# Kernel tuning notes

Hardware: AMD Instinct MI355X
Metric: run time of the kernel (lower is better)

The kernel has to match this reference:

```python
import jax, jax.numpy as jnp
import numpy as np

N = 100000
E = 800000
D_IN = 128
D_H = 128
D_OUT = 40
L = 16
ALPHA = 0.1
THETA = 0.5
BN_EPS = 1e-5


def setup_inputs() -> dict:
    key = jax.random.key(0)
    ks = jax.random.split(key, 8)
    x = jax.random.normal(ks[0], (N, D_IN), dtype=jnp.float32)
    edge_row = jax.random.randint(ks[1], (E,), 0, N, dtype=jnp.int32)
    edge_col = jax.random.randint(ks[2], (E,), 0, N, dtype=jnp.int32)
    edge_weight = jax.random.uniform(ks[3], (E,), dtype=jnp.float32) / 8.0  # ~normalized adj values
    W_in = jax.random.normal(ks[4], (D_IN, D_H), dtype=jnp.float32) / np.sqrt(D_IN)
    b_in = jnp.zeros((D_H,), jnp.float32)
    conv_W = jax.random.normal(ks[5], (L, D_H, D_H), dtype=jnp.float32) / np.sqrt(D_H)
    bn_gamma = jnp.ones((L, D_H), jnp.float32)
    bn_beta = jnp.zeros((L, D_H), jnp.float32)
    W_out = jax.random.normal(ks[6], (D_H, D_OUT), dtype=jnp.float32) / np.sqrt(D_H)
    b_out = jnp.zeros((D_OUT,), jnp.float32)
    return {"x": x, "edge_weight": edge_weight, "W_in": W_in, "b_in": b_in,
            "conv_W": conv_W, "bn_gamma": bn_gamma, "bn_beta": bn_beta,
            "W_out": W_out, "b_out": b_out,
            "edge_row": edge_row, "edge_col": edge_col}


def reference(x, edge_weight, W_in, b_in, conv_W, bn_gamma, bn_beta, W_out, b_out, edge_row, edge_col):
    # input linear + relu (dropout p=0 -> identity)
    x0 = jax.nn.relu(x @ W_in + b_in)            # [N, D_H]
    # GCN2Conv beta coefficients: log(theta/layer + 1), layer = 1..L
    betas = jnp.log(THETA / jnp.arange(1, L + 1, dtype=jnp.float32) + 1.0)

    def spmm(h):
        # out[i] = sum_{e: row[e]=i} w[e] * h[col[e]]
        msgs = edge_weight[:, None] * h[edge_col]     # [E, D_H]
        return jax.ops.segment_sum(msgs, edge_row, num_segments=N)

    def layer(h, params):
        W, g, bb, beta = params
        a = spmm(h)                                   # propagate
        a = (1.0 - ALPHA) * a + ALPHA * x0            # initial-residual mix
        a = (1.0 - beta) * a + beta * (a @ W)         # shared-weights identity mapping
        mu = jnp.mean(a, axis=0)                      # BatchNorm1d (training stats)
        var = jnp.var(a, axis=0)
        a = (a - mu) * jax.lax.rsqrt(var + BN_EPS) * g + bb
        a = a + h                                     # residual
        return jax.nn.relu(a), None

    xL, _ = jax.lax.scan(layer, x0, (conv_W, bn_gamma, bn_beta, betas))
    return xL @ W_out + b_out                         # [N, D_OUT]
```

## Files before the change

### kernel.cpp

```cpp
#include <hip/hip_runtime.h>
#include <math.h>

#define NN 100000
#define EE 800000
#define DH 128
#define NL 16
#define GEMM_GRID 1563
#define SG_GRID 782
#define NSLOT 32
#define WROWS 12500

typedef __bf16 bf16x8 __attribute__((ext_vector_type(8)));
typedef float f32x4 __attribute__((ext_vector_type(4)));

__global__ void k_hist(const int* __restrict__ row, int* __restrict__ cnt) {
    int e = blockIdx.x * 256 + threadIdx.x;
    if (e < EE) atomicAdd(&cnt[row[e]], 1);
}

__global__ void k_scan1(const int* __restrict__ cnt, int* __restrict__ rp, int* __restrict__ part) {
    __shared__ int buf[512];
    int tid = threadIdx.x;
    int i = blockIdx.x * 512 + tid;
    int v = (i < NN) ? cnt[i] : 0;
    buf[tid] = v;
    __syncthreads();
    for (int off = 1; off < 512; off <<= 1) {
        int x = (tid >= off) ? buf[tid - off] : 0;
        __syncthreads();
        buf[tid] += x;
        __syncthreads();
    }
    if (i < NN) rp[i] = buf[tid] - v;
    if (tid == 511) part[blockIdx.x] = buf[511];
}

__global__ void k_scan2(int* __restrict__ part, int nparts) {
    __shared__ int buf[256];
    int tid = threadIdx.x;
    int v = (tid < nparts) ? part[tid] : 0;
    buf[tid] = v;
    __syncthreads();
    for (int off = 1; off < 256; off <<= 1) {
        int x = (tid >= off) ? buf[tid - off] : 0;
        __syncthreads();
        buf[tid] += x;
        __syncthreads();
    }
    if (tid < nparts) part[tid] = buf[tid] - v;
}

__global__ void k_scan3(int* __restrict__ rp, const int* __restrict__ part) {
    int i = blockIdx.x * 512 + threadIdx.x;
    if (i < NN) rp[i] += part[blockIdx.x];
    if (i == 0) rp[NN] = EE;
}

__global__ void k_dhist(const int* __restrict__ cnt, int* __restrict__ dbin) {
    __shared__ int lb[64];
    int tid = threadIdx.x;
    if (tid < 64) lb[tid] = 0;
    __syncthreads();
    int i = blockIdx.x * 256 + tid;
    if (i < NN) {
        int d = cnt[i];
        if (d > 63) d = 63;
        atomicAdd(&lb[63 - d], 1);
    }
    __syncthreads();
    if (tid < 64 && lb[tid]) atomicAdd(&dbin[tid], lb[tid]);
}

__global__ void k_pscan(const int* __restrict__ dbin, int* __restrict__ dpre) {
    if (threadIdx.x == 0) {
        int s = 0;
        for (int i = 0; i < 64; ++i) { dpre[i] = s; s += dbin[i]; }
    }
}

__global__ void k_pscatter(const int* __restrict__ cnt, const int* __restrict__ dpre,
                           int* __restrict__ dfil, int* __restrict__ perm) {
    __shared__ int lcnt[64], lbase[64];
    int tid = threadIdx.x;
    if (tid < 64) lcnt[tid] = 0;
    __syncthreads();
    int i = blockIdx.x * 256 + tid;
    int b = 0, loc = 0;
    bool ok = (i < NN);
    if (ok) {
        int d = cnt[i];
        if (d > 63) d = 63;
        b = 63 - d;
        loc = atomicAdd(&lcnt[b], 1);
    }
    __syncthreads();
    if (tid < 64 && lcnt[tid]) lbase[tid] = atomicAdd(&dfil[tid], lcnt[tid]);
    __syncthreads();
    if (ok) perm[dpre[b] + lbase[b] + loc] = i;
}

__global__ void k_iperm(const int* __restrict__ perm, const int* __restrict__ cnt,
                        int* __restrict__ iperm, int* __restrict__ cnt2) {
    int i = blockIdx.x * 256 + threadIdx.x;
    if (i < NN) {
        int p = perm[i];
        iperm[p] = i;
        cnt2[i] = cnt[p];
    }
}

__global__ void k_fill(const int* __restrict__ row, const int* __restrict__ col,
                       const float* __restrict__ w, const int* __restrict__ rp,
                       const int* __restrict__ iperm,
                       int* __restrict__ fil, int2* __restrict__ ep) {
    int b = blockIdx.x;
    int win = b & 7;
    int e = (b >> 3) * 256 + threadIdx.x;
    if (e >= EE) return;
    int r = iperm[row[e]];
    if (r / WROWS != win) return;
    int pos = rp[r] + atomicAdd(&fil[r], 1);
    ep[pos] = make_int2(iperm[col[e]], __float_as_int(0.9f * w[e]));
}

__global__ void k_prep_w(const float* __restrict__ convW, const float* __restrict__ Win,
                         __bf16* __restrict__ Bhi, __bf16* __restrict__ Blo) {
    int l = blockIdx.x;
    const float* W;
    float beta, ob;
    if (l < NL) {
        beta = logf(0.5f / (float)(l + 1) + 1.0f);
        ob = 1.0f - beta;
        W = convW + (size_t)l * DH * DH;
    } else {
        beta = 1.0f;
        ob = 0.0f;
        W = Win;
    }
    __bf16* bh = Bhi + (size_t)l * DH * DH;
    __bf16* bl = Blo + (size_t)l * DH * DH;
    for (int i = threadIdx.x; i < DH * DH; i += 256) {
        int k = i >> 7, j = i & 127;
        float v = beta * W[i] + ((k == j) ? ob : 0.f);
        __bf16 hv = (__bf16)v;
        int t = j >> 4, n = j & 15, ks = k >> 5, quad = (k >> 3) & 3, e = k & 7;
        int off = ((t * 4 + ks) * 64 + quad * 16 + n) * 8 + e;
        bh[off] = hv;
        bl[off] = (__bf16)(v - (float)hv);
    }
}

__global__ void k_prep_out(const float* __restrict__ Wout, __bf16* __restrict__ Bhi, __bf16* __restrict__ Blo) {
    for (int i = threadIdx.x; i < DH * 48; i += 256) {
        int k = i / 48, j = i % 48;
        float v = (j < 40) ? Wout[k * 40 + j] : 0.f;
        __bf16 hv = (__bf16)v;
        int t = j >> 4, n = j & 15, ks = k >> 5, quad = (k >> 3) & 3, e = k & 7;
        int off = ((t * 4 + ks) * 64 + quad * 16 + n) * 8 + e;
        Bhi[off] = hv;
        Blo[off] = (__bf16)(v - (float)hv);
    }
}

__device__ inline void split8(const float* p, bf16x8& hi, bf16x8& lo) {
    f32x4 v0 = *(const f32x4*)p;
    f32x4 v1 = *(const f32x4*)(p + 4);
#pragma unroll
    for (int j = 0; j < 4; ++j) {
        __bf16 h0 = (__bf16)v0[j];
        hi[j] = h0;
        lo[j] = (__bf16)(v0[j] - (float)h0);
        __bf16 h1 = (__bf16)v1[j];
        hi[4 + j] = h1;
        lo[4 + j] = (__bf16)(v1[j] - (float)h1);
    }
}

#define MFMA(a, b, c) __builtin_amdgcn_mfma_f32_16x16x32_bf16(a, b, c, 0, 0, 0)

__device__ inline float dec_scale(unsigned int sc4, int ks) {
    return __uint_as_float(((sc4 >> (8 * ks)) & 0xffu) << 23);
}

#define DEC_DW(dw, wsv, a0, a1, a2, a3)                         \
    {                                                           \
        a0 = fmaf(wsv, (float)((dw)&0xffu), a0);                \
        a1 = fmaf(wsv, (float)(((dw) >> 8) & 0xffu), a1);       \
        a2 = fmaf(wsv, (float)(((dw) >> 16) & 0xffu), a2);      \
        a3 = fmaf(wsv, (float)((dw) >> 24), a3);                \
    }

#define EDGE_FMA(S4, W, RA, RB)                                       \
    {                                                                 \
        float _w = (W);                                               \
        float _w0 = _w * dec_scale(S4, 0);                            \
        float _w1 = _w * dec_scale(S4, 1);                            \
        float _w2 = _w * dec_scale(S4, 2);                            \
        float _w3 = _w * dec_scale(S4, 3);                            \
        sw0 += _w0; sw1 += _w1; sw2 += _w2; sw3 += _w3;               \
        DEC_DW((RA).x, _w0, acc[0][0], acc[0][1], acc[0][2], acc[0][3]); \
        DEC_DW((RA).y, _w0, acc[0][4], acc[0][5], acc[0][6], acc[0][7]); \
        DEC_DW((RA).z, _w1, acc[1][0], acc[1][1], acc[1][2], acc[1][3]); \
        DEC_DW((RA).w, _w1, acc[1][4], acc[1][5], acc[1][6], acc[1][7]); \
        DEC_DW((RB).x, _w2, acc[2][0], acc[2][1], acc[2][2], acc[2][3]); \
        DEC_DW((RB).y, _w2, acc[2][4], acc[2][5], acc[2][6], acc[2][7]); \
        DEC_DW((RB).z, _w3, acc[3][0], acc[3][1], acc[3][2], acc[3][3]); \
        DEC_DW((RB).w, _w3, acc[3][4], acc[3][5], acc[3][6], acc[3][7]); \
    }

__global__ void k_cvt8(const __bf16* __restrict__ src, unsigned char* __restrict__ q8,
                       unsigned char* __restrict__ sc) {
    int t = blockIdx.x * 256 + threadIdx.x;
    if (t >= NN * 4) return;
    int node = t >> 2, ks = t & 3;
    const __bf16* p = src + (size_t)node * DH + ks * 32;
    float v[32];
    float mx = 0.f;
#pragma unroll
    for (int i = 0; i < 4; ++i) {
        bf16x8 b = *(const bf16x8*)(p + i * 8);
#pragma unroll
        for (int c = 0; c < 8; ++c) {
            float f = (float)b[c];
            v[i * 8 + c] = f;
            mx = fmaxf(mx, fabsf(f));
        }
    }
    unsigned int em = (__float_as_uint(mx) >> 23) & 0xffu;
    unsigned int eb;
    float sinv;
    if (em < 7) { eb = 0; sinv = 0.f; }
    else { eb = em - 6; sinv = __uint_as_float((254 - eb) << 23); }
    sc[(size_t)node * 4 + ks] = (unsigned char)eb;
    unsigned char* bp = q8 + (size_t)node * 128 + (ks >> 1) * 64 + (ks & 1) * 8;
#pragma unroll
    for (int q = 0; q < 4; ++q) {
        uint2 w;
        w.x = 0; w.y = 0;
#pragma unroll
        for (int c = 0; c < 4; ++c) {
            unsigned int q0 = (unsigned int)rintf(fminf(fmaf(v[q * 8 + c], sinv, 128.f), 255.f));
            unsigned int q1 = (unsigned int)rintf(fminf(fmaf(v[q * 8 + 4 + c], sinv, 128.f), 255.f));
            w.x |= q0 << (8 * c);
            w.y |= q1 << (8 * c);
        }
        *(uint2*)(bp + q * 16) = w;
    }
}

__global__ __launch_bounds__(512, 4) void k_spmm_gemm(const unsigned char* __restrict__ hin8,
                                                      const unsigned char* __restrict__ hinsc,
                                                      const unsigned char* __restrict__ x08,
                                                      const unsigned char* __restrict__ x0sc,
                                                      const int* __restrict__ rp, const int2* __restrict__ ep,
                                                      __bf16* __restrict__ aout,
                                                      const __bf16* __restrict__ Bhi, const __bf16* __restrict__ Blo,
                                                      float* __restrict__ stats32) {
    __shared__ __bf16 Bs[2 * DH * DH];
    __shared__ float red[2][8][DH];
    int tid = threadIdx.x;
    {
        const f32x4* sh = (const f32x4*)Bhi;
        const f32x4* sl = (const f32x4*)Blo;
        f32x4* dh = (f32x4*)Bs;
        f32x4* dl = (f32x4*)(Bs + DH * DH);
#pragma unroll
        for (int i = 0; i < 4; ++i) {
            dh[tid + i * 512] = sh[tid + i * 512];
            dl[tid + i * 512] = sl[tid + i * 512];
        }
    }

    int wave = tid >> 6, lane = tid & 63;
    int n = lane & 15, quad = lane >> 4;
    int r0 = blockIdx.x * 128 + wave * 16;
    int node = r0 + n;
    int nc = (node < NN) ? node : (NN - 1);

    float acc[4][8];
#pragma unroll
    for (int ks = 0; ks < 4; ++ks)
#pragma unroll
        for (int c = 0; c < 8; ++c) acc[ks][c] = 0.f;
    float sw0 = 0.f, sw1 = 0.f, sw2 = 0.f, sw3 = 0.f;

    unsigned xs4 = *(const unsigned*)&x0sc[(size_t)nc * 4];
    const unsigned char* xb = x08 + (size_t)nc * 128 + quad * 16;
    uint4 xa = *(const uint4*)xb;
    uint4 xc = *(const uint4*)(xb + 64);

    int s = 0, e = 0;
    if (node < NN) { s = rp[node]; e = rp[node + 1]; }
    int cnt = e - s;
    int npairs = cnt >> 1;

    const unsigned char* hb = hin8 + quad * 16;

    int2 cP0, cP1, fP0, fP1;
    unsigned cS0, cS1;
    uint4 cA0, cB0, cA1, cB1;
    if (npairs > 0) {
        cP0 = ep[s]; cP1 = ep[s + 1];
        cS0 = *(const unsigned*)&hinsc[(size_t)cP0.x * 4];
        cS1 = *(const unsigned*)&hinsc[(size_t)cP1.x * 4];
        const unsigned char* b0 = hb + (size_t)cP0.x * 128;
        const unsigned char* b1 = hb + (size_t)cP1.x * 128;
        cA0 = *(const uint4*)b0; cB0 = *(const uint4*)(b0 + 64);
        cA1 = *(const uint4*)b1; cB1 = *(const uint4*)(b1 + 64);
        int jf = s + 2; if (jf > EE - 2) jf = EE - 2;
        fP0 = ep[jf]; fP1 = ep[jf + 1];
    }

    EDGE_FMA(xs4, 0.1f, xa, xc);

    int j = s;
    for (int it = 0; it < npairs; ++it) {
        int j2 = j + 4; if (j2 > EE - 2) j2 = EE - 2;
        int2 eN0 = ep[j2], eN1 = ep[j2 + 1];
        unsigned tS0 = *(const unsigned*)&hinsc[(size_t)fP0.x * 4];
        unsigned tS1 = *(const unsigned*)&hinsc[(size_t)fP1.x * 4];
        const unsigned char* b0 = hb + (size_t)fP0.x * 128;
        const unsigned char* b1 = hb + (size_t)fP1.x * 128;
        uint4 tA0 = *(const uint4*)b0, tB0 = *(const uint4*)(b0 + 64);
        uint4 tA1 = *(const uint4*)b1, tB1 = *(const uint4*)(b1 + 64);
        EDGE_FMA(cS0, __int_as_float(cP0.y), cA0, cB0);
        EDGE_FMA(cS1, __int_as_float(cP1.y), cA1, cB1);
        cP0 = fP0; cP1 = fP1; fP0 = eN0; fP1 = eN1;
        cS0 = tS0; cS1 = tS1;
        cA0 = tA0; cB0 = tB0; cA1 = tA1; cB1 = tB1;
        j += 2;
    }
    if (cnt & 1) {
        int2 pe = ep[e - 1];
        unsigned s4 = *(const unsigned*)&hinsc[(size_t)pe.x * 4];
        const unsigned char* bp = hb + (size_t)pe.x * 128;
        uint4 ra = *(const uint4*)bp, rb = *(const uint4*)(bp + 64);
        EDGE_FMA(s4, __int_as_float(pe.y), ra, rb);
    }

    bf16x8 av[4];
    {
        float sws[4] = {sw0, sw1, sw2, sw3};
#pragma unroll
        for (int ks = 0; ks < 4; ++ks)
#pragma unroll
            for (int c = 0; c < 8; ++c)
                av[ks][c] = (__bf16)(acc[ks][c] - 128.0f * sws[ks]);
    }

    __syncthreads();

    f32x4 gacc[8];
#pragma unroll
    for (int t = 0; t < 8; ++t) gacc[t] = (f32x4){0.f, 0.f, 0.f, 0.f};

#pragma unroll
    for (int ks = 0; ks < 4; ++ks) {
#pragma unroll
        for (int t = 0; t < 8; ++t) {
            int base = ((t * 4 + ks) * 64 + lane) * 8;
            bf16x8 bh = *(const bf16x8*)&Bs[base];
            bf16x8 bl = *(const bf16x8*)&Bs[DH * DH + base];
            gacc[t] = MFMA(av[ks], bh, gacc[t]);
            gacc[t] = MFMA(av[ks], bl, gacc[t]);
        }
    }

#pragma unroll
    for (int t = 0; t < 8; ++t) {
        float sm = 0.f, qq = 0.f;
#pragma unroll
        for (int r = 0; r < 4; ++r) {
            int row = r0 + quad * 4 + r;
            float v = gacc[t][r];
            if (row < NN) {
                aout[(size_t)row * DH + t * 16 + n] = (__bf16)v;
                sm += v;
                qq += v * v;
            }
        }
        sm += __shfl_xor(sm, 16); sm += __shfl_xor(sm, 32);
        qq += __shfl_xor(qq, 16); qq += __shfl_xor(qq, 32);
        if (quad == 0) {
            red[0][wave][t * 16 + n] = sm;
            red[1][wave][t * 16 + n] = qq;
        }
    }
    __syncthreads();
    if (tid < 256) {
        int which = tid >> 7, jj = tid & 127;
        float tot = 0.f;
#pragma unroll
        for (int w = 0; w < 8; ++w) tot += red[which][w][jj];
        atomicAdd(&stats32[(size_t)(blockIdx.x & (NSLOT - 1)) * 256 + tid], tot);
    }
}

__global__ __launch_bounds__(512, 4) void k_lin_in(const float* __restrict__ X, const int* __restrict__ perm,
                                                   const __bf16* __restrict__ Bhi, const __bf16* __restrict__ Blo,
                                                   const float* __restrict__ bin, __bf16* __restrict__ x0) {
    __shared__ __bf16 Bs[2 * DH * DH];
    int tid = threadIdx.x;
    {
        const f32x4* sh = (const f32x4*)Bhi;
        const f32x4* sl = (const f32x4*)Blo;
        f32x4* dh = (f32x4*)Bs;
        f32x4* dl = (f32x4*)(Bs + DH * DH);
#pragma unroll
        for (int i = 0; i < 4; ++i) {
            dh[tid + i * 512] = sh[tid + i * 512];
            dl[tid + i * 512] = sl[tid + i * 512];
        }
    }
    __syncthreads();

    int wave = tid >> 6, lane = tid & 63;
    int n = lane & 15, quad = lane >> 4;
    int r0 = blockIdx.x * 128 + wave * 16;
    int arow = r0 + n;
    if (arow > NN - 1) arow = NN - 1;
    const float* pa = X + (size_t)perm[arow] * DH + quad * 8;

    f32x4 acc[8];
#pragma unroll
    for (int t = 0; t < 8; ++t) acc[t] = (f32x4){0.f, 0.f, 0.f, 0.f};

#pragma unroll
    for (int ks = 0; ks < 4; ++ks) {
        bf16x8 ah, al;
        split8(pa + ks * 32, ah, al);
#pragma unroll
        for (int t = 0; t < 8; ++t) {
            int base = ((t * 4 + ks) * 64 + lane) * 8;
            bf16x8 bh = *(const bf16x8*)&Bs[base];
            bf16x8 bl = *(const bf16x8*)&Bs[DH * DH + base];
            acc[t] = MFMA(ah, bh, acc[t]);
            acc[t] = MFMA(al, bh, acc[t]);
            acc[t] = MFMA(ah, bl, acc[t]);
        }
    }

#pragma unroll
    for (int t = 0; t < 8; ++t) {
        float bj = bin[t * 16 + n];
#pragma unroll
        for (int r = 0; r < 4; ++r) {
            int row = r0 + quad * 4 + r;
            if (row < NN) {
                float v = fmaxf(acc[t][r] + bj, 0.f);
                x0[(size_t)row * DH + t * 16 + n] = (__bf16)v;
            }
        }
    }
}

__global__ __launch_bounds__(256) void k_gemm_out(const __bf16* __restrict__ A, const int* __restrict__ perm,
                                                  const __bf16* __restrict__ Bhi, const __bf16* __restrict__ Blo,
                                                  const float* __restrict__ bout, float* __restrict__ out) {
    __shared__ __bf16 Bs[2 * 48 * DH];
    int tid = threadIdx.x;
    {
        const f32x4* sh = (const f32x4*)Bhi;
        const f32x4* sl = (const f32x4*)Blo;
        f32x4* dh = (f32x4*)Bs;
        f32x4* dl = (f32x4*)(Bs + 48 * DH);
#pragma unroll
        for (int i = 0; i < 3; ++i) {
            dh[tid + i * 256] = sh[tid + i * 256];
            dl[tid + i * 256] = sl[tid + i * 256];
        }
    }
    __syncthreads();

    int wave = tid >> 6, lane = tid & 63;
    int n = lane & 15, quad = lane >> 4;
    int r0 = blockIdx.x * 64 + wave * 16;
    int arow = r0 + n;
    if (arow > NN - 1) arow = NN - 1;
    const __bf16* pa = A + (size_t)arow * DH + quad * 8;

    f32x4 acc[3];
#pragma unroll
    for (int t = 0; t < 3; ++t) acc[t] = (f32x4){0.f, 0.f, 0.f, 0.f};

#pragma unroll
    for (int ks = 0; ks < 4; ++ks) {
        bf16x8 av = *(const bf16x8*)(pa + ks * 32);
#pragma unroll
        for (int t = 0; t < 3; ++t) {
            int base = ((t * 4 + ks) * 64 + lane) * 8;
            bf16x8 bh = *(const bf16x8*)&Bs[base];
            bf16x8 bl = *(const bf16x8*)&Bs[48 * DH + base];
            acc[t] = MFMA(av, bh, acc[t]);
            acc[t] = MFMA(av, bl, acc[t]);
        }
    }

    int prow[4];
#pragma unroll
    for (int r = 0; r < 4; ++r) {
        int row = r0 + quad * 4 + r;
        prow[r] = (row < NN) ? perm[row] : 0;
    }

#pragma unroll
    for (int t = 0; t < 3; ++t) {
        int j = t * 16 + n;
        float bj = (j < 40) ? bout[j] : 0.f;
#pragma unroll
        for (int r = 0; r < 4; ++r) {
            int row = r0 + quad * 4 + r;
            if (row < NN && j < 40) out[(size_t)prow[r] * 40 + j] = acc[t][r] + bj;
        }
    }
}

__global__ __launch_bounds__(256) void k_update(const __bf16* __restrict__ a, const __bf16* __restrict__ hin,
                                                __bf16* __restrict__ hout,
                                                unsigned char* __restrict__ h8, unsigned char* __restrict__ hsc,
                                                const float* __restrict__ stats32,
                                                const float* __restrict__ gamma, const float* __restrict__ bbeta) {
    __shared__ float scb[DH], shb[DH];
    int tid = threadIdx.x;
    if (tid < DH) {
        float s = 0.f, q = 0.f;
#pragma unroll
        for (int sl = 0; sl < NSLOT; ++sl) {
            s += stats32[(size_t)sl * 256 + tid];
            q += stats32[(size_t)sl * 256 + 128 + tid];
        }
        float mu = s * (1.0f / NN);
        float var = q * (1.0f / NN) - mu * mu;
        if (var < 0.f) var = 0.f;
        float sc = gamma[tid] * rsqrtf(var + 1e-5f);
        scb[tid] = sc;
        shb[tid] = bbeta[tid] - mu * sc;
    }
    __syncthreads();

    int idx = blockIdx.x * 256 + tid;
    int sub = idx & 15;
    int j0 = sub * 8;
    bf16x8 av = ((const bf16x8*)a)[idx];
    bf16x8 hv = ((const bf16x8*)hin)[idx];
    bf16x8 o;
    float vv[8];
    float mx = 0.f;
#pragma unroll
    for (int c = 0; c < 8; ++c) {
        int j = j0 + c;
        float v = fmaxf(fmaf((float)av[c], scb[j], shb[j]) + (float)hv[c], 0.f);
        vv[c] = v;
        mx = fmaxf(mx, v);
        o[c] = (__bf16)v;
    }
    ((bf16x8*)hout)[idx] = o;

    mx = fmaxf(mx, __shfl_xor(mx, 1));
    mx = fmaxf(mx, __shfl_xor(mx, 2));
    unsigned int em = (__float_as_uint(mx) >> 23) & 0xffu;
    unsigned int eb;
    float sinv;
    if (em < 7) { eb = 0; sinv = 0.f; }
    else { eb = em - 6; sinv = __uint_as_float((254 - eb) << 23); }
    if ((tid & 3) == 0) hsc[(size_t)(idx >> 4) * 4 + (sub >> 2)] = (unsigned char)eb;
    uint2 pk;
    pk.x = 0; pk.y = 0;
#pragma unroll
    for (int c = 0; c < 4; ++c) {
        unsigned int q0 = (unsigned int)rintf(fminf(fmaf(vv[c], sinv, 128.f), 255.f));
        unsigned int q1 = (unsigned int)rintf(fminf(fmaf(vv[4 + c], sinv, 128.f), 255.f));
        pk.x |= q0 << (8 * c);
        pk.y |= q1 << (8 * c);
    }
    unsigned wpos = ((sub >> 3) & 1) * 64 + (sub & 3) * 16 + ((sub >> 2) & 1) * 8;
    *(uint2*)&h8[(size_t)(idx >> 4) * 128 + wpos] = pk;
}

extern "C" void kernel_launch(void* const* d_in, const int* in_sizes, int n_in,
                              void* d_out, int out_size, void* d_ws, size_t ws_size,
                              hipStream_t stream) {
    const float* x = (const float*)d_in[0];
    const float* ew = (const float*)d_in[1];
    const float* Win = (const float*)d_in[2];
    const float* bin = (const float*)d_in[3];
    const float* convW = (const float*)d_in[4];
    const float* gamma = (const float*)d_in[5];
    const float* bbeta = (const float*)d_in[6];
    const float* Wout = (const float*)d_in[7];
    const float* bout = (const float*)d_in[8];
    const int* erow = (const int*)d_in[9];
    const int* ecol = (const int*)d_in[10];
    float* out = (float*)d_out;

    char* wsp = (char*)d_ws;
    size_t off = 0;
    auto alloc = [&](size_t bytes) -> void* {
        void* p = wsp + off;
        off += (bytes + 255) & ~(size_t)255;
        return p;
    };
    __bf16* x0 = (__bf16*)alloc((size_t)NN * DH * 2);
    __bf16* h = (__bf16*)alloc((size_t)NN * DH * 2);
    __bf16* a = (__bf16*)alloc((size_t)NN * DH * 2);
    unsigned char* x08 = (unsigned char*)alloc((size_t)NN * DH);
    unsigned char* h8 = (unsigned char*)alloc((size_t)NN * DH);
    unsigned char* x0sc = (unsigned char*)alloc((size_t)NN * 4);
    unsigned char* hsc = (unsigned char*)alloc((size_t)NN * 4);
    int* rp = (int*)alloc((NN + 1) * 4);
    int* perm = (int*)alloc((size_t)NN * 4);
    int* iperm = (int*)alloc((size_t)NN * 4);
    int* cnt2 = (int*)alloc((size_t)NN * 4);
    int* dpre = (int*)alloc(64 * 4);
    size_t zero_bytes = (size_t)NN * 4 + (size_t)NN * 4 + (size_t)NL * NSLOT * 256 * 4 + 128 * 4;
    int* cnt = (int*)alloc(zero_bytes);
    int* fil = cnt + NN;
    float* stats32 = (float*)(fil + NN);
    int* dbin = (int*)(stats32 + (size_t)NL * NSLOT * 256);
    int* dfil = dbin + 64;
    int2* ep = (int2*)alloc((size_t)EE * 8);
    int* part = (int*)alloc(256 * 4);
    __bf16* Bhi = (__bf16*)alloc((size_t)(NL + 1) * DH * DH * 2);
    __bf16* Blo = (__bf16*)alloc((size_t)(NL + 1) * DH * DH * 2);
    __bf16* Bohi = (__bf16*)alloc((size_t)DH * 48 * 2);
    __bf16* Bolo = (__bf16*)alloc((size_t)DH * 48 * 2);

    hipMemsetAsync(cnt, 0, zero_bytes, stream);

    k_hist<<<3125, 256, 0, stream>>>(erow, cnt);
    k_dhist<<<391, 256, 0, stream>>>(cnt, dbin);
    k_pscan<<<1, 64, 0, stream>>>(dbin, dpre);
    k_pscatter<<<391, 256, 0, stream>>>(cnt, dpre, dfil, perm);
    k_iperm<<<391, 256, 0, stream>>>(perm, cnt, iperm, cnt2);
    k_scan1<<<196, 512, 0, stream>>>(cnt2, rp, part);
    k_scan2<<<1, 256, 0, stream>>>(part, 196);
    k_scan3<<<196, 512, 0, stream>>>(rp, part);
    k_fill<<<25000, 256, 0, stream>>>(erow, ecol, ew, rp, iperm, fil, ep);

    k_prep_w<<<NL + 1, 256, 0, stream>>>(convW, Win, Bhi, Blo);
    k_prep_out<<<1, 256, 0, stream>>>(Wout, Bohi, Bolo);

    k_lin_in<<<SG_GRID, 512, 0, stream>>>(x, perm, Bhi + (size_t)NL * DH * DH, Blo + (size_t)NL * DH * DH, bin, x0);
    k_cvt8<<<1563, 256, 0, stream>>>(x0, x08, x0sc);

    for (int l = 0; l < NL; ++l) {
        const unsigned char* hin8 = (l == 0) ? x08 : h8;
        const unsigned char* hinsc = (l == 0) ? x0sc : hsc;
        const __bf16* hin = (l == 0) ? x0 : h;
        float* st = stats32 + (size_t)l * NSLOT * 256;
        k_spmm_gemm<<<SG_GRID, 512, 0, stream>>>(hin8, hinsc, x08, x0sc, rp, ep, a,
                                                 Bhi + (size_t)l * DH * DH, Blo + (size_t)l * DH * DH, st);
        k_update<<<6250, 256, 0, stream>>>(a, hin, h, h8, hsc, st, gamma + l * DH, bbeta + l * DH);
    }
    k_gemm_out<<<GEMM_GRID, 256, 0, stream>>>(h, perm, Bohi, Bolo, bout, out);
}
```

Before: 1.154 ms.

## Store intermediate activations as 8-bit quantized, fuse x0 quantization, simplify edge fill

The spmm+gemm kernel now writes its per-layer output as 8-bit block-scaled values with per-32-column exponent scales instead of bf16, and the update kernel dequantizes them. This halves the intermediate write and read traffic every layer. The input linear kernel now quantizes x0 directly, so the separate conversion kernel is removed. The edge fill drops its 8-window row partitioning in favour of a single pass with nontemporal loads and stores. The extra quantization adds error to the pre-BatchNorm activations, though the statistics are still computed from full-precision values.

```diff
diff --git a/kernel.cpp b/kernel.cpp
--- a/kernel.cpp
+++ b/kernel.cpp
@@ -8,14 +8,13 @@
 #define GEMM_GRID 1563
 #define SG_GRID 782
 #define NSLOT 32
-#define WROWS 12500
 
 typedef __bf16 bf16x8 __attribute__((ext_vector_type(8)));
 typedef float f32x4 __attribute__((ext_vector_type(4)));
 
 __global__ void k_hist(const int* __restrict__ row, int* __restrict__ cnt) {
     int e = blockIdx.x * 256 + threadIdx.x;
-    if (e < EE) atomicAdd(&cnt[row[e]], 1);
+    if (e < EE) atomicAdd(&cnt[__builtin_nontemporal_load(&row[e])], 1);
 }
 
 __global__ void k_scan1(const int* __restrict__ cnt, int* __restrict__ rp, int* __restrict__ part) {
@@ -113,14 +112,15 @@
                        const float* __restrict__ w, const int* __restrict__ rp,
                        const int* __restrict__ iperm,
                        int* __restrict__ fil, int2* __restrict__ ep) {
-    int b = blockIdx.x;
-    int win = b & 7;
-    int e = (b >> 3) * 256 + threadIdx.x;
+    int e = blockIdx.x * 256 + threadIdx.x;
     if (e >= EE) return;
-    int r = iperm[row[e]];
-    if (r / WROWS != win) return;
+    int r = iperm[__builtin_nontemporal_load(&row[e])];
+    int c = iperm[__builtin_nontemporal_load(&col[e])];
+    float wv = 0.9f * __builtin_nontemporal_load(&w[e]);
     int pos = rp[r] + atomicAdd(&fil[r], 1);
-    ep[pos] = make_int2(iperm[col[e]], __float_as_int(0.9f * w[e]));
+    unsigned long long v = (unsigned long long)(unsigned)c |
+                           ((unsigned long long)(unsigned)__float_as_int(wv) << 32);
+    __builtin_nontemporal_store(v, (unsigned long long*)&ep[pos]);
 }
 
 __global__ void k_prep_w(const float* __restrict__ convW, const float* __restrict__ Win,
@@ -208,52 +208,12 @@
         DEC_DW((RB).w, _w3, acc[3][4], acc[3][5], acc[3][6], acc[3][7]); \
     }
 
-__global__ void k_cvt8(const __bf16* __restrict__ src, unsigned char* __restrict__ q8,
-                       unsigned char* __restrict__ sc) {
-    int t = blockIdx.x * 256 + threadIdx.x;
-    if (t >= NN * 4) return;
-    int node = t >> 2, ks = t & 3;
-    const __bf16* p = src + (size_t)node * DH + ks * 32;
-    float v[32];
-    float mx = 0.f;
-#pragma unroll
-    for (int i = 0; i < 4; ++i) {
-        bf16x8 b = *(const bf16x8*)(p + i * 8);
-#pragma unroll
-        for (int c = 0; c < 8; ++c) {
-            float f = (float)b[c];
-            v[i * 8 + c] = f;
-            mx = fmaxf(mx, fabsf(f));
-        }
-    }
-    unsigned int em = (__float_as_uint(mx) >> 23) & 0xffu;
-    unsigned int eb;
-    float sinv;
-    if (em < 7) { eb = 0; sinv = 0.f; }
-    else { eb = em - 6; sinv = __uint_as_float((254 - eb) << 23); }
-    sc[(size_t)node * 4 + ks] = (unsigned char)eb;
-    unsigned char* bp = q8 + (size_t)node * 128 + (ks >> 1) * 64 + (ks & 1) * 8;
-#pragma unroll
-    for (int q = 0; q < 4; ++q) {
-        uint2 w;
-        w.x = 0; w.y = 0;
-#pragma unroll
-        for (int c = 0; c < 4; ++c) {
-            unsigned int q0 = (unsigned int)rintf(fminf(fmaf(v[q * 8 + c], sinv, 128.f), 255.f));
-            unsigned int q1 = (unsigned int)rintf(fminf(fmaf(v[q * 8 + 4 + c], sinv, 128.f), 255.f));
-            w.x |= q0 << (8 * c);
-            w.y |= q1 << (8 * c);
-        }
-        *(uint2*)(bp + q * 16) = w;
-    }
-}
-
 __global__ __launch_bounds__(512, 4) void k_spmm_gemm(const unsigned char* __restrict__ hin8,
                                                       const unsigned char* __restrict__ hinsc,
                                                       const unsigned char* __restrict__ x08,
                                                       const unsigned char* __restrict__ x0sc,
                                                       const int* __restrict__ rp, const int2* __restrict__ ep,
-                                                      __bf16* __restrict__ aout,
+                                                      unsigned char* __restrict__ a8, unsigned char* __restrict__ asc,
                                                       const __bf16* __restrict__ Bhi, const __bf16* __restrict__ Blo,
                                                       float* __restrict__ stats32) {
     __shared__ __bf16 Bs[2 * DH * DH];
@@ -366,15 +326,48 @@
         }
     }
 
+    float m[4][4];
+#pragma unroll
+    for (int r = 0; r < 4; ++r)
+#pragma unroll
+        for (int g = 0; g < 4; ++g)
+            m[r][g] = fmaxf(fabsf(gacc[2 * g][r]), fabsf(gacc[2 * g + 1][r]));
+#pragma unroll
+    for (int d = 1; d <= 8; d <<= 1)
+#pragma unroll
+        for (int r = 0; r < 4; ++r)
+#pragma unroll
+            for (int g = 0; g < 4; ++g)
+                m[r][g] = fmaxf(m[r][g], __shfl_xor(m[r][g], d));
+    unsigned ebu[4];
+    float sinv[4][4];
+#pragma unroll
+    for (int r = 0; r < 4; ++r) {
+        unsigned u32 = 0;
+#pragma unroll
+        for (int g = 0; g < 4; ++g) {
+            unsigned em = (__float_as_uint(m[r][g]) >> 23) & 0xffu;
+            unsigned eb;
+            float si;
+            if (em < 7) { eb = 0; si = 0.f; }
+            else { eb = em - 6; si = __uint_as_float((254 - eb) << 23); }
+            u32 |= eb << (8 * g);
+            sinv[r][g] = si;
+        }
+        ebu[r] = u32;
+    }
+
 #pragma unroll
     for (int t = 0; t < 8; ++t) {
         float sm = 0.f, qq = 0.f;
+        int wb = (t >> 2) * 64 + ((((t & 1) << 1) | (n >> 3))) * 16 + ((t >> 1) & 1) * 8 + (n & 7);
 #pragma unroll
         for (int r = 0; r < 4; ++r) {
             int row = r0 + quad * 4 + r;
             float v = gacc[t][r];
             if (row < NN) {
-                aout[(size_t)row * DH + t * 16 + n] = (__bf16)v;
+                unsigned qv = (unsigned)rintf(fminf(fmaf(v, sinv[r][t >> 1], 128.f), 255.f));
+                a8[(size_t)row * 128 + wb] = (unsigned char)qv;
                 sm += v;
                 qq += v * v;
             }
@@ -386,6 +379,13 @@
             red[1][wave][t * 16 + n] = qq;
         }
     }
+    if (n == 0) {
+#pragma unroll
+        for (int r = 0; r < 4; ++r) {
+            int row = r0 + quad * 4 + r;
+            if (row < NN) *(unsigned*)&asc[(size_t)row * 4] = ebu[r];
+        }
+    }
     __syncthreads();
     if (tid < 256) {
         int which = tid >> 7, jj = tid & 127;
@@ -398,7 +398,8 @@
 
 __global__ __launch_bounds__(512, 4) void k_lin_in(const float* __restrict__ X, const int* __restrict__ perm,
                                                    const __bf16* __restrict__ Bhi, const __bf16* __restrict__ Blo,
-                                                   const float* __restrict__ bin, __bf16* __restrict__ x0) {
+                                                   const float* __restrict__ bin, __bf16* __restrict__ x0,
+                                                   unsigned char* __restrict__ x08, unsigned char* __restrict__ xsc) {
     __shared__ __bf16 Bs[2 * DH * DH];
     int tid = threadIdx.x;
     {
@@ -445,11 +446,64 @@
         float bj = bin[t * 16 + n];
 #pragma unroll
         for (int r = 0; r < 4; ++r) {
+            float v = fmaxf(acc[t][r] + bj, 0.f);
+            acc[t][r] = v;
+            int row = r0 + quad * 4 + r;
+            if (row < NN) x0[(size_t)row * DH + t * 16 + n] = (__bf16)v;
+        }
+    }
+
+    float m[4][4];
+#pragma unroll
+    for (int r = 0; r < 4; ++r)
+#pragma unroll
+        for (int g = 0; g < 4; ++g) {
+            float v0 = (float)(__bf16)acc[2 * g][r];
+            float v1 = (float)(__bf16)acc[2 * g + 1][r];
+            m[r][g] = fmaxf(fabsf(v0), fabsf(v1));
+        }
+#pragma unroll
+    for (int d = 1; d <= 8; d <<= 1)
+#pragma unroll
+        for (int r = 0; r < 4; ++r)
+#pragma unroll
+            for (int g = 0; g < 4; ++g)
+                m[r][g] = fmaxf(m[r][g], __shfl_xor(m[r][g], d));
+    unsigned ebu[4];
+    float sinv[4][4];
+#pragma unroll
+    for (int r = 0; r < 4; ++r) {
+        unsigned u32 = 0;
+#pragma unroll
+        for (int g = 0; g < 4; ++g) {
+            unsigned em = (__float_as_uint(m[r][g]) >> 23) & 0xffu;
+            unsigned eb;
+            float si;
+            if (em < 7) { eb = 0; si = 0.f; }
+            else { eb = em - 6; si = __uint_as_float((254 - eb) << 23); }
+            u32 |= eb << (8 * g);
+            sinv[r][g] = si;
+        }
+        ebu[r] = u32;
+    }
+#pragma unroll
+    for (int t = 0; t < 8; ++t) {
+        int wb = (t >> 2) * 64 + ((((t & 1) << 1) | (n >> 3))) * 16 + ((t >> 1) & 1) * 8 + (n & 7);
+#pragma unroll
+        for (int r = 0; r < 4; ++r) {
             int row = r0 + quad * 4 + r;
             if (row < NN) {
-                float v = fmaxf(acc[t][r] + bj, 0.f);
-                x0[(size_t)row * DH + t * 16 + n] = (__bf16)v;
+                float v = (float)(__bf16)acc[t][r];
+                unsigned qv = (unsigned)rintf(fminf(fmaf(v, sinv[r][t >> 1], 128.f), 255.f));
+                x08[(size_t)row * 128 + wb] = (unsigned char)qv;
             }
+        }
+    }
+    if (n == 0) {
+#pragma unroll
+        for (int r = 0; r < 4; ++r) {
+            int row = r0 + quad * 4 + r;
+            if (row < NN) *(unsigned*)&xsc[(size_t)row * 4] = ebu[r];
         }
     }
 }
@@ -515,7 +569,9 @@
     }
 }
 
-__global__ __launch_bounds__(256) void k_update(const __bf16* __restrict__ a, const __bf16* __restrict__ hin,
+__global__ __launch_bounds__(256) void k_update(const unsigned char* __restrict__ a8,
+                                                const unsigned char* __restrict__ asc,
+                                                const __bf16* __restrict__ hin,
                                                 __bf16* __restrict__ hout,
                                                 unsigned char* __restrict__ h8, unsigned char* __restrict__ hsc,
                                                 const float* __restrict__ stats32,
@@ -540,16 +596,21 @@
 
     int idx = blockIdx.x * 256 + tid;
     int sub = idx & 15;
+    int row = idx >> 4;
     int j0 = sub * 8;
-    bf16x8 av = ((const bf16x8*)a)[idx];
+    unsigned wpos = ((sub >> 3) & 1) * 64 + (sub & 3) * 16 + ((sub >> 2) & 1) * 8;
+    uint2 ua = *(const uint2*)&a8[(size_t)row * 128 + wpos];
+    float sA = dec_scale(*(const unsigned*)&asc[(size_t)row * 4], sub >> 2);
     bf16x8 hv = ((const bf16x8*)hin)[idx];
     bf16x8 o;
     float vv[8];
     float mx = 0.f;
 #pragma unroll
     for (int c = 0; c < 8; ++c) {
+        unsigned byte = ((c < 4 ? (ua.x >> (8 * c)) : (ua.y >> (8 * (c - 4)))) & 0xffu);
+        float ad = ((float)byte - 128.f) * sA;
         int j = j0 + c;
-        float v = fmaxf(fmaf((float)av[c], scb[j], shb[j]) + (float)hv[c], 0.f);
+        float v = fmaxf(fmaf(ad, scb[j], shb[j]) + (float)hv[c], 0.f);
         vv[c] = v;
         mx = fmaxf(mx, v);
         o[c] = (__bf16)v;
@@ -563,7 +624,7 @@
     float sinv;
     if (em < 7) { eb = 0; sinv = 0.f; }
     else { eb = em - 6; sinv = __uint_as_float((254 - eb) << 23); }
-    if ((tid & 3) == 0) hsc[(size_t)(idx >> 4) * 4 + (sub >> 2)] = (unsigned char)eb;
+    if ((tid & 3) == 0) hsc[(size_t)row * 4 + (sub >> 2)] = (unsigned char)eb;
     uint2 pk;
     pk.x = 0; pk.y = 0;
 #pragma unroll
@@ -573,8 +634,7 @@
         pk.x |= q0 << (8 * c);
         pk.y |= q1 << (8 * c);
     }
-    unsigned wpos = ((sub >> 3) & 1) * 64 + (sub & 3) * 16 + ((sub >> 2) & 1) * 8;
-    *(uint2*)&h8[(size_t)(idx >> 4) * 128 + wpos] = pk;
+    *(uint2*)&h8[(size_t)row * 128 + wpos] = pk;
 }
 
 extern "C" void kernel_launch(void* const* d_in, const int* in_sizes, int n_in,
@@ -602,7 +662,8 @@
     };
     __bf16* x0 = (__bf16*)alloc((size_t)NN * DH * 2);
     __bf16* h = (__bf16*)alloc((size_t)NN * DH * 2);
-    __bf16* a = (__bf16*)alloc((size_t)NN * DH * 2);
+    unsigned char* a8 = (unsigned char*)alloc((size_t)NN * DH);
+    unsigned char* asc = (unsigned char*)alloc((size_t)NN * 4);
     unsigned char* x08 = (unsigned char*)alloc((size_t)NN * DH);
     unsigned char* h8 = (unsigned char*)alloc((size_t)NN * DH);
     unsigned char* x0sc = (unsigned char*)alloc((size_t)NN * 4);
@@ -635,22 +696,22 @@
     k_scan1<<<196, 512, 0, stream>>>(cnt2, rp, part);
     k_scan2<<<1, 256, 0, stream>>>(part, 196);
     k_scan3<<<196, 512, 0, stream>>>(rp, part);
-    k_fill<<<25000, 256, 0, stream>>>(erow, ecol, ew, rp, iperm, fil, ep);
+    k_fill<<<3125, 256, 0, stream>>>(erow, ecol, ew, rp, iperm, fil, ep);
 
     k_prep_w<<<NL + 1, 256, 0, stream>>>(convW, Win, Bhi, Blo);
     k_prep_out<<<1, 256, 0, stream>>>(Wout, Bohi, Bolo);
 
-    k_lin_in<<<SG_GRID, 512, 0, stream>>>(x, perm, Bhi + (size_t)NL * DH * DH, Blo + (size_t)NL * DH * DH, bin, x0);
-    k_cvt8<<<1563, 256, 0, stream>>>(x0, x08, x0sc);
+    k_lin_in<<<SG_GRID, 512, 0, stream>>>(x, perm, Bhi + (size_t)NL * DH * DH, Blo + (size_t)NL * DH * DH,
+                                          bin, x0, x08, x0sc);
 
     for (int l = 0; l < NL; ++l) {
         const unsigned char* hin8 = (l == 0) ? x08 : h8;
         const unsigned char* hinsc = (l == 0) ? x0sc : hsc;
         const __bf16* hin = (l == 0) ? x0 : h;
         float* st = stats32 + (size_t)l * NSLOT * 256;
-        k_spmm_gemm<<<SG_GRID, 512, 0, stream>>>(hin8, hinsc, x08, x0sc, rp, ep, a,
+        k_spmm_gemm<<<SG_GRID, 512, 0, stream>>>(hin8, hinsc, x08, x0sc, rp, ep, a8, asc,
                                                  Bhi + (size_t)l * DH * DH, Blo + (size_t)l * DH * DH, st);
-        k_update<<<6250, 256, 0, stream>>>(a, hin, h, h8, hsc, st, gamma + l * DH, bbeta + l * DH);
+        k_update<<<6250, 256, 0, stream>>>(a8, asc, hin, h, h8, hsc, st, gamma + l * DH, bbeta + l * DH);
     }
     k_gemm_out<<<GEMM_GRID, 256, 0, stream>>>(h, perm, Bohi, Bolo, bout, out);
 }
```

Result: slower. 1.193 ms (+3.3%).
